# Performance work log

Hardware: AMD Instinct MI355X
Metric: run time of the kernel (lower is better)

Reference implementation:

```python
import jax, jax.numpy as jnp
import numpy as np

H, NH, NKV, HD, S, B = 4096, 32, 8, 128, 2048, 1
QMAX = 127.0  # int8 symmetric


def fake_quant(x, axis=None):
    """Symmetric int8 fake quantization with straight-through estimator.
    axis=None -> per-tensor dynamic scale; axis=int -> per-channel along that axis."""
    if axis is None:
        amax = jnp.max(jnp.abs(x))
    else:
        amax = jnp.max(jnp.abs(x), axis=axis, keepdims=True)
    scale = jnp.maximum(amax, 1e-8) / QMAX
    q = jnp.clip(jnp.round(x / scale), -QMAX - 1, QMAX) * scale
    return x + jax.lax.stop_gradient(q - x)


def quant_linear(x, w):
    # weight: per-output-channel quant (reduce over in-features axis=1);
    # activation: per-tensor dynamic quant
    xq = fake_quant(x)
    wq = fake_quant(w, axis=1)
    return jnp.einsum('bsh,oh->bso', xq, wq)


def rotate_half(x):
    x1, x2 = jnp.split(x, 2, axis=-1)
    return jnp.concatenate([-x2, x1], axis=-1)


def apply_rope(q, k, cos, sin):
    # q: [B,NH,S,HD], k: [B,NKV,S,HD], cos/sin: [B,S,HD]
    cos = cos[:, None, :, :]
    sin = sin[:, None, :, :]
    return q * cos + rotate_half(q) * sin, k * cos + rotate_half(k) * sin


def setup_inputs() -> dict:
    key = jax.random.key(0)
    ks = jax.random.split(key, 6)
    hidden_states = jax.random.normal(ks[0], (B, S, H), jnp.float32)
    # additive causal mask
    neg = jnp.finfo(jnp.float32).min
    mask = jnp.where(jnp.tril(jnp.ones((S, S), bool)), 0.0, neg)
    attention_mask = jnp.broadcast_to(mask, (B, 1, S, S)).astype(jnp.float32)
    # rotary cos/sin
    inv_freq = 1.0 / (10000.0 ** (jnp.arange(0, HD, 2, dtype=jnp.float32) / HD))
    t = jnp.arange(S, dtype=jnp.float32)
    freqs = jnp.outer(t, inv_freq)                     # [S, HD/2]
    emb = jnp.concatenate([freqs, freqs], axis=-1)     # [S, HD]
    cos = jnp.broadcast_to(jnp.cos(emb), (B, S, HD))
    sin = jnp.broadcast_to(jnp.sin(emb), (B, S, HD))
    sc = 0.02
    wq = jax.random.normal(ks[1], (H, H), jnp.float32) * sc
    wk = jax.random.normal(ks[2], (NKV * HD, H), jnp.float32) * sc
    wv = jax.random.normal(ks[3], (NKV * HD, H), jnp.float32) * sc
    wo = jax.random.normal(ks[4], (H, H), jnp.float32) * sc
    return {"hidden_states": hidden_states, "attention_mask": attention_mask,
            "cos": cos, "sin": sin, "wq": wq, "wk": wk, "wv": wv, "wo": wo}


def reference(hidden_states, attention_mask, cos, sin, wq, wk, wv, wo):
    b, s, _ = hidden_states.shape
    scaling = HD ** -0.5
    q = quant_linear(hidden_states, wq).reshape(b, s, NH, HD).transpose(0, 2, 1, 3)
    k = quant_linear(hidden_states, wk).reshape(b, s, NKV, HD).transpose(0, 2, 1, 3)
    v = quant_linear(hidden_states, wv).reshape(b, s, NKV, HD).transpose(0, 2, 1, 3)
    q, k = apply_rope(q, k, cos, sin)
    groups = NH // NKV
    k = jnp.repeat(k, groups, axis=1)  # [B,NH,S,HD]
    v = jnp.repeat(v, groups, axis=1)
    # quantize before QK^T
    qq = fake_quant(q)
    kq = fake_quant(k)
    attn = jnp.einsum('bhqd,bhkd->bhqk', qq, kq) * scaling
    attn = attn + attention_mask
    attn = jnp.maximum(attn, jnp.finfo(attn.dtype).min)
    attn = jax.nn.softmax(attn.astype(jnp.float32), axis=-1).astype(q.dtype)
    # quantize before PV
    pq = fake_quant(attn)
    vq = fake_quant(v)
    out = jnp.einsum('bhqk,bhkd->bhqd', pq, vq)
    out = out.transpose(0, 2, 1, 3).reshape(b, s, NH * HD)
    out = quant_linear(out, wo)
    return out
```

## Files before the change

### kernel.cpp

```cpp
#include <hip/hip_runtime.h>
#include <cstdint>
#include <cstddef>


#define S_LEN   2048
#define HDIM    4096
#define NHEADS  32
#define NKVH    8
#define HEADD   128
#define QMAXF   127.0f
#define ROPE_BLOCKS 20480

typedef _Float16 half8  __attribute__((ext_vector_type(8)));
typedef float    floatx4 __attribute__((ext_vector_type(4)));

__device__ __forceinline__ float wave_max64(float v){
#pragma unroll
  for (int off = 32; off > 0; off >>= 1) v = fmaxf(v, __shfl_xor(v, off));
  return v;
}
__device__ __forceinline__ float grp16_max(float v){
#pragma unroll
  for (int off = 8; off > 0; off >>= 1) v = fmaxf(v, __shfl_xor(v, off));
  return v;
}
__device__ __forceinline__ float grp16_sum(float v){
#pragma unroll
  for (int off = 8; off > 0; off >>= 1) v += __shfl_xor(v, off);
  return v;
}
__device__ __forceinline__ void atomic_max_f(unsigned* p, float v){
  atomicMax(p, __float_as_uint(v));
}
__device__ __forceinline__ float q8(float x, float scale){
  return fminf(fmaxf(rintf(x / scale), -128.f), 127.f);
}
__device__ __forceinline__ void gload_lds16(const _Float16* g, _Float16* l){
  __builtin_amdgcn_global_load_lds((const __attribute__((address_space(1))) void*)g,
                                   (__attribute__((address_space(3))) void*)l, 16, 0, 0);
}

__device__ __forceinline__ void block_atomic_max(float m, unsigned* out){
  m = wave_max64(m);
  __shared__ float red[4];
  int wid = threadIdx.x >> 6;
  if ((threadIdx.x & 63) == 0) red[wid] = m;
  __syncthreads();
  if (threadIdx.x == 0)
    atomic_max_f(out, fmaxf(fmaxf(red[0], red[1]), fmaxf(red[2], red[3])));
}

__global__ void k_init(float* scal){ if (threadIdx.x < 16) scal[threadIdx.x] = 0.0f; }

__global__ void k_amax(const float* __restrict__ x, size_t n4, unsigned* __restrict__ out){
  size_t i = (size_t)blockIdx.x * blockDim.x + threadIdx.x;
  size_t stride = (size_t)gridDim.x * blockDim.x;
  float m = 0.f;
  for (; i < n4; i += stride){
    float4 v = ((const float4*)x)[i];
    m = fmaxf(m, fmaxf(fmaxf(fabsf(v.x), fabsf(v.y)), fmaxf(fabsf(v.z), fabsf(v.w))));
  }
  block_atomic_max(m, out);
}

__global__ void k_amax_v(const float* __restrict__ Y, unsigned* __restrict__ out){
  size_t i = (size_t)blockIdx.x * blockDim.x + threadIdx.x;
  size_t stride = (size_t)gridDim.x * blockDim.x;
  float m = 0.f;
  for (size_t e = i; e < (size_t)S_LEN * 1024; e += stride){
    size_t s = e >> 10; int c = (int)(e & 1023);
    m = fmaxf(m, fabsf(Y[s * 6144 + 5120 + c]));
  }
  block_atomic_max(m, out);
}

__global__ void k_quant(const float* __restrict__ x, _Float16* __restrict__ q,
                        size_t n4, const float* __restrict__ amax){
  float scale = fmaxf(*amax, 1e-8f) / QMAXF;
  size_t i = (size_t)blockIdx.x * blockDim.x + threadIdx.x;
  size_t stride = (size_t)gridDim.x * blockDim.x;
  for (; i < n4; i += stride){
    float4 v = ((const float4*)x)[i];
    union { _Float16 h[4]; uint2 u; } pk;
    pk.h[0] = (_Float16)q8(v.x, scale);
    pk.h[1] = (_Float16)q8(v.y, scale);
    pk.h[2] = (_Float16)q8(v.z, scale);
    pk.h[3] = (_Float16)q8(v.w, scale);
    ((uint2*)q)[i] = pk.u;
  }
}

__global__ __launch_bounds__(256) void k_quant_w(
    const float* __restrict__ wq, const float* __restrict__ wk,
    const float* __restrict__ wv, const float* __restrict__ wo,
    _Float16* __restrict__ Wall, _Float16* __restrict__ Wo,
    float* __restrict__ wsc)
{
  int row = blockIdx.x;
  const float* src; _Float16* dst;
  if (row < 4096)      { src = wq + (size_t)row * HDIM;          dst = Wall + (size_t)row * HDIM; }
  else if (row < 5120) { src = wk + (size_t)(row - 4096) * HDIM; dst = Wall + (size_t)row * HDIM; }
  else if (row < 6144) { src = wv + (size_t)(row - 5120) * HDIM; dst = Wall + (size_t)row * HDIM; }
  else                 { src = wo + (size_t)(row - 6144) * HDIM; dst = Wo + (size_t)(row - 6144) * HDIM; }
  float4 v[4]; float m = 0.f;
#pragma unroll
  for (int i = 0; i < 4; i++){
    v[i] = ((const float4*)src)[threadIdx.x + i * 256];
    m = fmaxf(m, fmaxf(fmaxf(fabsf(v[i].x), fabsf(v[i].y)), fmaxf(fabsf(v[i].z), fabsf(v[i].w))));
  }
  m = wave_max64(m);
  __shared__ float red[4];
  int wid = threadIdx.x >> 6;
  if ((threadIdx.x & 63) == 0) red[wid] = m;
  __syncthreads();
  float am = fmaxf(fmaxf(red[0], red[1]), fmaxf(red[2], red[3]));
  float scale = fmaxf(am, 1e-8f) / QMAXF;
  if (threadIdx.x == 0) wsc[row] = scale;
#pragma unroll
  for (int i = 0; i < 4; i++){
    union { _Float16 h[4]; uint2 u; } pk;
    pk.h[0] = (_Float16)q8(v[i].x, scale);
    pk.h[1] = (_Float16)q8(v[i].y, scale);
    pk.h[2] = (_Float16)q8(v[i].z, scale);
    pk.h[3] = (_Float16)q8(v[i].w, scale);
    ((uint2*)dst)[threadIdx.x + i * 256] = pk.u;
  }
}

__global__ __launch_bounds__(256) void k_rope(
    float* __restrict__ Y, const float* __restrict__ cosb,
    const float* __restrict__ sinb,
    float* __restrict__ qpart, float* __restrict__ kpart)
{
  int idx = blockIdx.x * 256 + threadIdx.x;
  int s = idx / (40 * 64);
  int rem = idx - s * 40 * 64;
  int head = rem >> 6;
  int d = rem & 63;
  size_t base = (size_t)s * 6144 + (head < 32 ? head * 128 : 4096 + (head - 32) * 128);
  float x1 = Y[base + d], x2 = Y[base + d + 64];
  float c1 = cosb[s * 128 + d],      s1 = sinb[s * 128 + d];
  float c2 = cosb[s * 128 + d + 64], s2 = sinb[s * 128 + d + 64];
  float o1 = x1 * c1 - x2 * s1;
  float o2 = x2 * c2 + x1 * s2;
  Y[base + d] = o1; Y[base + d + 64] = o2;
  float m = wave_max64(fmaxf(fabsf(o1), fabsf(o2)));
  __shared__ float wmax[4]; __shared__ int wisq[4];
  int wid = threadIdx.x >> 6;
  if ((threadIdx.x & 63) == 0){ wmax[wid] = m; wisq[wid] = (head < 32); }
  __syncthreads();
  if (threadIdx.x == 0){
    float qm = 0.f, km = 0.f;
#pragma unroll
    for (int w = 0; w < 4; w++){
      if (wisq[w]) qm = fmaxf(qm, wmax[w]); else km = fmaxf(km, wmax[w]);
    }
    qpart[blockIdx.x] = qm; kpart[blockIdx.x] = km;
  }
}

__global__ __launch_bounds__(256) void k_reduce_qk(
    const float* __restrict__ qpart, const float* __restrict__ kpart,
    float* __restrict__ scal)
{
  const float* src = blockIdx.x ? kpart : qpart;
  float m = 0.f;
  for (int i = threadIdx.x; i < ROPE_BLOCKS; i += 256) m = fmaxf(m, src[i]);
  m = wave_max64(m);
  __shared__ float red[4];
  int wid = threadIdx.x >> 6;
  if ((threadIdx.x & 63) == 0) red[wid] = m;
  __syncthreads();
  if (threadIdx.x == 0)
    scal[1 + blockIdx.x] = fmaxf(fmaxf(red[0], red[1]), fmaxf(red[2], red[3]));
}

__global__ __launch_bounds__(256) void k_quant_qk(
    const float* __restrict__ Y, _Float16* __restrict__ Qh,
    _Float16* __restrict__ Kh, const float* __restrict__ scal)
{
  int i = blockIdx.x * 256 + threadIdx.x;
  int s = i / 1280, c4 = i - s * 1280;
  int col = c4 * 4;
  float4 v = *(const float4*)(Y + (size_t)s * 6144 + col);
  float scale = fmaxf(col < 4096 ? scal[1] : scal[2], 1e-8f) / QMAXF;
  union { _Float16 h[4]; uint2 u; } pk;
  pk.h[0] = (_Float16)q8(v.x, scale);
  pk.h[1] = (_Float16)q8(v.y, scale);
  pk.h[2] = (_Float16)q8(v.z, scale);
  pk.h[3] = (_Float16)q8(v.w, scale);
  if (col < 4096) *(uint2*)(Qh + (size_t)s * 4096 + col) = pk.u;
  else            *(uint2*)(Kh + (size_t)s * 1024 + (col - 4096)) = pk.u;
}

__global__ __launch_bounds__(256) void k_quant_vt(
    const float* __restrict__ Y, _Float16* __restrict__ Vt,
    const float* __restrict__ scal)
{
  __shared__ _Float16 sT[64][72];
  const int s0 = blockIdx.x * 64, kvh = blockIdx.y, dh = blockIdx.z;
  const float scale = fmaxf(scal[3], 1e-8f) / QMAXF;
  const int d = threadIdx.x & 63, srow = threadIdx.x >> 6;
#pragma unroll
  for (int i = 0; i < 16; i++){
    int s = srow + i * 4;
    float v = Y[(size_t)(s0 + s) * 6144 + 5120 + kvh * 128 + dh * 64 + d];
    sT[d][s] = (_Float16)q8(v, scale);
  }
  __syncthreads();
  const int dr = threadIdx.x >> 2, j = threadIdx.x & 3;
  _Float16* dst = Vt + (size_t)kvh * HEADD * S_LEN + (size_t)(dh * 64 + dr) * S_LEN + s0 + j * 16;
  *(uint4*)(dst)     = *(const uint4*)(&sT[dr][j * 16]);
  *(uint4*)(dst + 8) = *(const uint4*)(&sT[dr][j * 16 + 8]);
}

__global__ __launch_bounds__(256) void k_gemm_nt(
    const _Float16* __restrict__ A, const _Float16* __restrict__ B,
    const float* __restrict__ amax_a, const float* __restrict__ sb,
    float* __restrict__ C, int M, int N, int K)
{
  __shared__ _Float16 sA[128 * 32];
  __shared__ _Float16 sB[128 * 32];
  const int m0 = blockIdx.x * 128;
  const int n0 = blockIdx.y * 128;
  const int tid = threadIdx.x;
  const int w = tid >> 6, lane = tid & 63;
  const int quad = lane >> 4, l16 = lane & 15;
  const int wm = (w & 1) * 64, wn = (w >> 1) * 64;
  floatx4 acc[4][4] = {};
  const int srow = w * 16 + (lane >> 2);
  const int scol = (lane & 3) * 8;
  const _Float16* gA0 = A + (size_t)(m0 + srow) * K + scol;
  const _Float16* gA1 = A + (size_t)(m0 + 64 + srow) * K + scol;
  const _Float16* gB0 = B + (size_t)(n0 + srow) * K + scol;
  const _Float16* gB1 = B + (size_t)(n0 + 64 + srow) * K + scol;
  _Float16* dA0 = sA + w * 512 + lane * 8;
  _Float16* dA1 = sA + 2048 + w * 512 + lane * 8;
  _Float16* dB0 = sB + w * 512 + lane * 8;
  _Float16* dB1 = sB + 2048 + w * 512 + lane * 8;

  for (int k0 = 0; k0 < K; k0 += 32){
    __syncthreads();
    gload_lds16(gA0 + k0, dA0);
    gload_lds16(gA1 + k0, dA1);
    gload_lds16(gB0 + k0, dB0);
    gload_lds16(gB1 + k0, dB1);
    __syncthreads();
    half8 af[4], bf[4];
#pragma unroll
    for (int i = 0; i < 4; i++){
      af[i] = *(const half8*)(sA + (wm + i * 16 + l16) * 32 + quad * 8);
      bf[i] = *(const half8*)(sB + (wn + i * 16 + l16) * 32 + quad * 8);
    }
#pragma unroll
    for (int i = 0; i < 4; i++)
#pragma unroll
      for (int j = 0; j < 4; j++)
        acc[i][j] = __builtin_amdgcn_mfma_f32_16x16x32_f16(af[i], bf[j], acc[i][j], 0, 0, 0);
  }
  const float sa = fmaxf(*amax_a, 1e-8f) / QMAXF;
#pragma unroll
  for (int i = 0; i < 4; i++){
    int row = m0 + wm + i * 16 + quad * 4;
#pragma unroll
    for (int j = 0; j < 4; j++){
      int col = n0 + wn + j * 16 + l16;
      float sc2 = sa * sb[col];
#pragma unroll
      for (int rr = 0; rr < 4; rr++)
        C[(size_t)(row + rr) * N + col] = acc[i][j][rr] * sc2;
    }
  }
}

__global__ __launch_bounds__(256) void k_attn(
    const _Float16* __restrict__ Qh,
    const _Float16* __restrict__ Kh,
    const _Float16* __restrict__ Vt,
    const float* __restrict__ scal,
    float* __restrict__ AO)
{
  const int h   = blockIdx.y;
  const int kvh = h >> 2;
  const int tid = threadIdx.x;
  const int wid = tid >> 6, lane = tid & 63;
  const int quad = lane >> 4, l16 = lane & 15;

  __shared__ _Float16 sK[64 * 136];
  __shared__ _Float16 sV[128 * 72];
  __shared__ _Float16 sP[4][16 * 72];

  const float s_q = fmaxf(scal[1], 1e-8f) / QMAXF;
  const float s_k = fmaxf(scal[2], 1e-8f) / QMAXF;
  const float s_v = fmaxf(scal[3], 1e-8f) / QMAXF;
  const float qkscale = s_q * s_k * 0.08838834764831845f;
  const float osc = s_v * (1.0f / QMAXF);

  for (int half = 0; half < 2; half++){
    const int qb = half ? (31 - blockIdx.x) : blockIdx.x;
    const int qrow = qb * 64 + wid * 16 + l16;
    half8 qf[4];
#pragma unroll
    for (int kk = 0; kk < 4; kk++)
      qf[kk] = *(const half8*)(Qh + (size_t)qrow * 4096 + h * 128 + kk * 32 + quad * 8);
    const int q_of_reg = qb * 64 + wid * 16 + quad * 4;

    float mrow[4] = { -__builtin_inff(), -__builtin_inff(), -__builtin_inff(), -__builtin_inff() };
    float lrow[4] = { 0.f, 0.f, 0.f, 0.f };

    for (int kt = 0; kt <= qb; ++kt){
      int r = tid >> 2, seg = tid & 3;
      const uint4* gK = (const uint4*)(Kh + (size_t)(kt * 64 + r) * 1024 + kvh * 128 + seg * 32);
      uint4 t0 = gK[0], t1 = gK[1], t2 = gK[2], t3 = gK[3];
      __syncthreads();
      { uint4* d1 = (uint4*)(sK + r * 136 + seg * 32); d1[0] = t0; d1[1] = t1; d1[2] = t2; d1[3] = t3; }
      __syncthreads();
      float sv[4][4];
      const bool diag = (kt == qb);
#pragma unroll
      for (int nt = 0; nt < 4; nt++){
        floatx4 c = {};
#pragma unroll
        for (int kk = 0; kk < 4; kk++){
          half8 bf = *(const half8*)(sK + (nt * 16 + l16) * 136 + kk * 32 + quad * 8);
          c = __builtin_amdgcn_mfma_f32_16x16x32_f16(qf[kk], bf, c, 0, 0, 0);
        }
        if (diag){
          int kpos = kt * 64 + nt * 16 + l16;
#pragma unroll
          for (int rr = 0; rr < 4; rr++)
            sv[nt][rr] = (kpos <= q_of_reg + rr) ? c[rr] * qkscale : -__builtin_inff();
        } else {
#pragma unroll
          for (int rr = 0; rr < 4; rr++) sv[nt][rr] = c[rr] * qkscale;
        }
      }
#pragma unroll
      for (int rr = 0; rr < 4; rr++){
        float lmax = fmaxf(fmaxf(sv[0][rr], sv[1][rr]), fmaxf(sv[2][rr], sv[3][rr]));
        float tmax = grp16_max(lmax);
        float mnew = fmaxf(mrow[rr], tmax);
        float lsum = 0.f;
#pragma unroll
        for (int nt = 0; nt < 4; nt++) lsum += __expf(sv[nt][rr] - mnew);
        lsum = grp16_sum(lsum);
        lrow[rr] = lrow[rr] * __expf(mrow[rr] - mnew) + lsum;
        mrow[rr] = mnew;
      }
    }

    float il[4];
#pragma unroll
    for (int rr = 0; rr < 4; rr++) il[rr] = QMAXF * __builtin_amdgcn_rcpf(lrow[rr]);

    floatx4 accO[8] = {};
    for (int kt = 0; kt <= qb; ++kt){
      int r = tid >> 2, seg = tid & 3;
      const uint4* gK = (const uint4*)(Kh + (size_t)(kt * 64 + r) * 1024 + kvh * 128 + seg * 32);
      uint4 t0 = gK[0], t1 = gK[1], t2 = gK[2], t3 = gK[3];
      int vr = tid >> 1, vh = tid & 1;
      const uint4* gV = (const uint4*)(Vt + (size_t)kvh * HEADD * S_LEN + (size_t)vr * S_LEN + kt * 64 + vh * 32);
      uint4 u0 = gV[0], u1 = gV[1], u2 = gV[2], u3 = gV[3];
      __syncthreads();
      { uint4* d1 = (uint4*)(sK + r * 136 + seg * 32); d1[0] = t0; d1[1] = t1; d1[2] = t2; d1[3] = t3; }
      { uint4* d2 = (uint4*)(sV + vr * 72 + vh * 32);  d2[0] = u0; d2[1] = u1; d2[2] = u2; d2[3] = u3; }
      __syncthreads();
      const bool diag = (kt == qb);
#pragma unroll
      for (int nt = 0; nt < 4; nt++){
        floatx4 c = {};
#pragma unroll
        for (int kk = 0; kk < 4; kk++){
          half8 bf = *(const half8*)(sK + (nt * 16 + l16) * 136 + kk * 32 + quad * 8);
          c = __builtin_amdgcn_mfma_f32_16x16x32_f16(qf[kk], bf, c, 0, 0, 0);
        }
        int kpos = kt * 64 + nt * 16 + l16;
#pragma unroll
        for (int rr = 0; rr < 4; rr++){
          float pq = fminf(rintf(__expf(c[rr] * qkscale - mrow[rr]) * il[rr]), 127.f);
          if (diag && kpos > q_of_reg + rr) pq = 0.f;
          sP[wid][(quad * 4 + rr) * 72 + nt * 16 + l16] = (_Float16)pq;
        }
      }
      __syncthreads();
      half8 pf0 = *(const half8*)(&sP[wid][l16 * 72 + quad * 8]);
      half8 pf1 = *(const half8*)(&sP[wid][l16 * 72 + 32 + quad * 8]);
#pragma unroll
      for (int dt = 0; dt < 8; dt++){
        half8 b0 = *(const half8*)(sV + (dt * 16 + l16) * 72 + quad * 8);
        half8 b1 = *(const half8*)(sV + (dt * 16 + l16) * 72 + 32 + quad * 8);
        accO[dt] = __builtin_amdgcn_mfma_f32_16x16x32_f16(pf0, b0, accO[dt], 0, 0, 0);
        accO[dt] = __builtin_amdgcn_mfma_f32_16x16x32_f16(pf1, b1, accO[dt], 0, 0, 0);
      }
    }

#pragma unroll
    for (int dt = 0; dt < 8; dt++){
      int col = h * 128 + dt * 16 + l16;
#pragma unroll
      for (int rr = 0; rr < 4; rr++)
        AO[(size_t)(q_of_reg + rr) * 4096 + col] = accO[dt][rr] * osc;
    }
  }
}

extern "C" void kernel_launch(void* const* d_in, const int* in_sizes, int n_in,
                              void* d_out, int out_size, void* d_ws, size_t ws_size,
                              hipStream_t stream)
{
  const float* hidden = (const float*)d_in[0];
  const float* cosb = (const float*)d_in[2];
  const float* sinb = (const float*)d_in[3];
  const float* wq = (const float*)d_in[4];
  const float* wk = (const float*)d_in[5];
  const float* wv = (const float*)d_in[6];
  const float* wo = (const float*)d_in[7];
  float* out = (float*)d_out;

  char* ws = (char*)d_ws;
  size_t off = 0;
  auto alloc = [&](size_t bytes){ size_t o = off; off += (bytes + 255) & ~(size_t)255; return o; };
  float*    scal  = (float*)   (ws + alloc(64));
  float*    wsc   = (float*)   (ws + alloc(10240 * 4));
  float*    qpart = (float*)   (ws + alloc(ROPE_BLOCKS * 4));
  float*    kpart = (float*)   (ws + alloc(ROPE_BLOCKS * 4));
  _Float16* Wall  = (_Float16*)(ws + alloc((size_t)6144 * 4096 * 2));
  _Float16* Wo    = (_Float16*)(ws + alloc((size_t)4096 * 4096 * 2));
  _Float16* Xq    = (_Float16*)(ws + alloc((size_t)2048 * 4096 * 2));
  float*    Y     = (float*)   (ws + alloc((size_t)2048 * 6144 * 4));
  _Float16* Qh  = Xq;
  _Float16* Kh  = Wall;
  _Float16* Vt  = Wall + (size_t)2048 * 1024;
  float*    AO  = Y;
  _Float16* AOq = (_Float16*)((char*)Y + (size_t)2048 * 4096 * 4);

  unsigned* su = (unsigned*)scal;

  k_init<<<dim3(1), dim3(64), 0, stream>>>(scal);
  k_quant_w<<<dim3(10240), dim3(256), 0, stream>>>(wq, wk, wv, wo, Wall, Wo, wsc);
  k_amax<<<dim3(256), dim3(256), 0, stream>>>(hidden, (size_t)(2048 * 4096 / 4), su + 0);
  k_quant<<<dim3(2048), dim3(256), 0, stream>>>(hidden, Xq, (size_t)(2048 * 4096 / 4), scal + 0);
  k_gemm_nt<<<dim3(16, 48), dim3(256), 0, stream>>>(Xq, Wall, scal + 0, wsc, Y, 2048, 6144, 4096);
  k_rope<<<dim3(ROPE_BLOCKS), dim3(256), 0, stream>>>(Y, cosb, sinb, qpart, kpart);
  k_reduce_qk<<<dim3(2), dim3(256), 0, stream>>>(qpart, kpart, scal);
  k_amax_v<<<dim3(256), dim3(256), 0, stream>>>(Y, su + 3);
  k_quant_qk<<<dim3(10240), dim3(256), 0, stream>>>(Y, Qh, Kh, scal);
  k_quant_vt<<<dim3(32, 8, 2), dim3(256), 0, stream>>>(Y, Vt, scal);
  k_attn<<<dim3(16, 32), dim3(256), 0, stream>>>(Qh, Kh, Vt, scal, AO);
  k_amax<<<dim3(256), dim3(256), 0, stream>>>(AO, (size_t)(2048 * 4096 / 4), su + 4);
  k_quant<<<dim3(2048), dim3(256), 0, stream>>>(AO, AOq, (size_t)(2048 * 4096 / 4), scal + 4);
  k_gemm_nt<<<dim3(16, 32), dim3(256), 0, stream>>>(AOq, Wo, scal + 4, wsc + 6144, out, 2048, 4096, 4096);
}
```

Before: 683.9 us.

## Restructure attention: two heads per block, transposed MFMA, double-buffered K/V prefetch

The attention kernel now has each block process two query heads that share one KV head, so each K/V tile loaded into shared memory is reused for both heads. The QK product is computed transposed (K as the A operand), which leaves P in registers in the layout the 16x16x16 PV MFMA expects and removes the sP shared-memory round trip and its extra barrier. Row reductions use cross-quad shuffles, and K/V tiles are double-buffered with register prefetch of the next tile. The grid is halved, and register pressure roughly doubles for accumulators, with launch bounds asking for 2 blocks per CU.

```diff
diff --git a/kernel.cpp b/kernel.cpp
--- a/kernel.cpp
+++ b/kernel.cpp
@@ -12,21 +12,12 @@
 #define ROPE_BLOCKS 20480
 
 typedef _Float16 half8  __attribute__((ext_vector_type(8)));
+typedef _Float16 half4  __attribute__((ext_vector_type(4)));
 typedef float    floatx4 __attribute__((ext_vector_type(4)));
 
 __device__ __forceinline__ float wave_max64(float v){
 #pragma unroll
   for (int off = 32; off > 0; off >>= 1) v = fmaxf(v, __shfl_xor(v, off));
-  return v;
-}
-__device__ __forceinline__ float grp16_max(float v){
-#pragma unroll
-  for (int off = 8; off > 0; off >>= 1) v = fmaxf(v, __shfl_xor(v, off));
-  return v;
-}
-__device__ __forceinline__ float grp16_sum(float v){
-#pragma unroll
-  for (int off = 8; off > 0; off >>= 1) v += __shfl_xor(v, off);
   return v;
 }
 __device__ __forceinline__ void atomic_max_f(unsigned* p, float v){
@@ -273,134 +264,182 @@
   }
 }
 
-__global__ __launch_bounds__(256) void k_attn(
+__global__ __launch_bounds__(256, 2) void k_attn(
     const _Float16* __restrict__ Qh,
     const _Float16* __restrict__ Kh,
     const _Float16* __restrict__ Vt,
     const float* __restrict__ scal,
     float* __restrict__ AO)
 {
-  const int h   = blockIdx.y;
-  const int kvh = h >> 2;
+  const int h0  = blockIdx.y * 2;
+  const int kvh = h0 >> 2;
   const int tid = threadIdx.x;
   const int wid = tid >> 6, lane = tid & 63;
   const int quad = lane >> 4, l16 = lane & 15;
 
-  __shared__ _Float16 sK[64 * 136];
-  __shared__ _Float16 sV[128 * 72];
-  __shared__ _Float16 sP[4][16 * 72];
+  __shared__ _Float16 sK[2][64 * 136];
+  __shared__ _Float16 sV[2][128 * 72];
 
   const float s_q = fmaxf(scal[1], 1e-8f) / QMAXF;
   const float s_k = fmaxf(scal[2], 1e-8f) / QMAXF;
   const float s_v = fmaxf(scal[3], 1e-8f) / QMAXF;
   const float qkscale = s_q * s_k * 0.08838834764831845f;
   const float osc = s_v * (1.0f / QMAXF);
-
-  for (int half = 0; half < 2; half++){
-    const int qb = half ? (31 - blockIdx.x) : blockIdx.x;
+  const float NEGINF = -__builtin_inff();
+
+  const int kr_ = tid >> 2, ks_ = tid & 3;
+  const int vr_ = tid >> 1, vh_ = tid & 1;
+  const _Float16* gK0 = Kh + (size_t)kr_ * 1024 + kvh * 128 + ks_ * 32;
+  const _Float16* gV0 = Vt + (size_t)kvh * HEADD * S_LEN + (size_t)vr_ * S_LEN + vh_ * 32;
+
+  for (int hf = 0; hf < 2; hf++){
+    const int qb = hf ? 31 - (int)blockIdx.x : (int)blockIdx.x;
+    const int nk = qb + 1;
     const int qrow = qb * 64 + wid * 16 + l16;
-    half8 qf[4];
-#pragma unroll
-    for (int kk = 0; kk < 4; kk++)
-      qf[kk] = *(const half8*)(Qh + (size_t)qrow * 4096 + h * 128 + kk * 32 + quad * 8);
-    const int q_of_reg = qb * 64 + wid * 16 + quad * 4;
-
-    float mrow[4] = { -__builtin_inff(), -__builtin_inff(), -__builtin_inff(), -__builtin_inff() };
-    float lrow[4] = { 0.f, 0.f, 0.f, 0.f };
-
-    for (int kt = 0; kt <= qb; ++kt){
-      int r = tid >> 2, seg = tid & 3;
-      const uint4* gK = (const uint4*)(Kh + (size_t)(kt * 64 + r) * 1024 + kvh * 128 + seg * 32);
-      uint4 t0 = gK[0], t1 = gK[1], t2 = gK[2], t3 = gK[3];
+    const int qloc = wid * 16 + l16;
+
+    half8 qf[2][4];
+#pragma unroll
+    for (int hh = 0; hh < 2; hh++)
+#pragma unroll
+      for (int kk = 0; kk < 4; kk++)
+        qf[hh][kk] = *(const half8*)(Qh + (size_t)qrow * 4096 + (h0 + hh) * 128 + kk * 32 + quad * 8);
+
+    float mh[2] = { NEGINF, NEGINF };
+    float lh[2] = { 0.f, 0.f };
+
+    uint4 kpre[4];
+    {
+      const uint4* g = (const uint4*)gK0;
+#pragma unroll
+      for (int j = 0; j < 4; j++) kpre[j] = g[j];
+    }
+    __syncthreads();
+    for (int kt = 0; kt < nk; ++kt){
+      const int b = kt & 1;
+      { uint4* d = (uint4*)(sK[b] + kr_ * 136 + ks_ * 32);
+#pragma unroll
+        for (int j = 0; j < 4; j++) d[j] = kpre[j]; }
       __syncthreads();
-      { uint4* d1 = (uint4*)(sK + r * 136 + seg * 32); d1[0] = t0; d1[1] = t1; d1[2] = t2; d1[3] = t3; }
+      if (kt + 1 < nk){
+        const uint4* g = (const uint4*)(gK0 + (size_t)(kt + 1) * 65536);
+#pragma unroll
+        for (int j = 0; j < 4; j++) kpre[j] = g[j];
+      }
+      const bool diag = (kt == qb);
+      floatx4 c0[4], c1[4];
+#pragma unroll
+      for (int mt = 0; mt < 4; mt++){
+        c0[mt] = (floatx4){0.f,0.f,0.f,0.f}; c1[mt] = (floatx4){0.f,0.f,0.f,0.f};
+#pragma unroll
+        for (int kk = 0; kk < 4; kk++){
+          half8 a = *(const half8*)(sK[b] + (mt * 16 + l16) * 136 + kk * 32 + quad * 8);
+          c0[mt] = __builtin_amdgcn_mfma_f32_16x16x32_f16(a, qf[0][kk], c0[mt], 0, 0, 0);
+          c1[mt] = __builtin_amdgcn_mfma_f32_16x16x32_f16(a, qf[1][kk], c1[mt], 0, 0, 0);
+        }
+      }
+#pragma unroll
+      for (int mt = 0; mt < 4; mt++)
+#pragma unroll
+        for (int rr = 0; rr < 4; rr++){
+          bool ok = !diag || (mt * 16 + quad * 4 + rr <= qloc);
+          c0[mt][rr] = ok ? c0[mt][rr] * qkscale : NEGINF;
+          c1[mt][rr] = ok ? c1[mt][rr] * qkscale : NEGINF;
+        }
+#pragma unroll
+      for (int hh = 0; hh < 2; hh++){
+        floatx4* c = hh ? c1 : c0;
+        float vmax = NEGINF;
+#pragma unroll
+        for (int mt = 0; mt < 4; mt++)
+#pragma unroll
+          for (int rr = 0; rr < 4; rr++) vmax = fmaxf(vmax, c[mt][rr]);
+        vmax = fmaxf(vmax, __shfl_xor(vmax, 16));
+        vmax = fmaxf(vmax, __shfl_xor(vmax, 32));
+        float mnew = fmaxf(mh[hh], vmax);
+        float sum = 0.f;
+#pragma unroll
+        for (int mt = 0; mt < 4; mt++)
+#pragma unroll
+          for (int rr = 0; rr < 4; rr++) sum += __expf(c[mt][rr] - mnew);
+        sum += __shfl_xor(sum, 16);
+        sum += __shfl_xor(sum, 32);
+        lh[hh] = lh[hh] * __expf(mh[hh] - mnew) + sum;
+        mh[hh] = mnew;
+      }
+    }
+    float il[2] = { QMAXF * __builtin_amdgcn_rcpf(lh[0]),
+                    QMAXF * __builtin_amdgcn_rcpf(lh[1]) };
+
+    floatx4 accO[2][8] = {};
+    uint4 kpre2[4], vpre2[4];
+    {
+      const uint4* g = (const uint4*)gK0;
+      const uint4* v = (const uint4*)gV0;
+#pragma unroll
+      for (int j = 0; j < 4; j++){ kpre2[j] = g[j]; vpre2[j] = v[j]; }
+    }
+    __syncthreads();
+    for (int kt = 0; kt < nk; ++kt){
+      const int b = kt & 1;
+      { uint4* d = (uint4*)(sK[b] + kr_ * 136 + ks_ * 32);
+        uint4* e = (uint4*)(sV[b] + vr_ * 72 + vh_ * 32);
+#pragma unroll
+        for (int j = 0; j < 4; j++){ d[j] = kpre2[j]; e[j] = vpre2[j]; } }
       __syncthreads();
-      float sv[4][4];
+      if (kt + 1 < nk){
+        const uint4* g = (const uint4*)(gK0 + (size_t)(kt + 1) * 65536);
+        const uint4* v = (const uint4*)(gV0 + (kt + 1) * 64);
+#pragma unroll
+        for (int j = 0; j < 4; j++){ kpre2[j] = g[j]; vpre2[j] = v[j]; }
+      }
       const bool diag = (kt == qb);
-#pragma unroll
-      for (int nt = 0; nt < 4; nt++){
-        floatx4 c = {};
+      floatx4 c0[4], c1[4];
+#pragma unroll
+      for (int mt = 0; mt < 4; mt++){
+        c0[mt] = (floatx4){0.f,0.f,0.f,0.f}; c1[mt] = (floatx4){0.f,0.f,0.f,0.f};
 #pragma unroll
         for (int kk = 0; kk < 4; kk++){
-          half8 bf = *(const half8*)(sK + (nt * 16 + l16) * 136 + kk * 32 + quad * 8);
-          c = __builtin_amdgcn_mfma_f32_16x16x32_f16(qf[kk], bf, c, 0, 0, 0);
+          half8 a = *(const half8*)(sK[b] + (mt * 16 + l16) * 136 + kk * 32 + quad * 8);
+          c0[mt] = __builtin_amdgcn_mfma_f32_16x16x32_f16(a, qf[0][kk], c0[mt], 0, 0, 0);
+          c1[mt] = __builtin_amdgcn_mfma_f32_16x16x32_f16(a, qf[1][kk], c1[mt], 0, 0, 0);
         }
-        if (diag){
-          int kpos = kt * 64 + nt * 16 + l16;
-#pragma unroll
-          for (int rr = 0; rr < 4; rr++)
-            sv[nt][rr] = (kpos <= q_of_reg + rr) ? c[rr] * qkscale : -__builtin_inff();
-        } else {
-#pragma unroll
-          for (int rr = 0; rr < 4; rr++) sv[nt][rr] = c[rr] * qkscale;
+      }
+      half4 pk[2][4];
+#pragma unroll
+      for (int hh = 0; hh < 2; hh++){
+        floatx4* c = hh ? c1 : c0;
+#pragma unroll
+        for (int mt = 0; mt < 4; mt++){
+          half4 p;
+#pragma unroll
+          for (int rr = 0; rr < 4; rr++){
+            bool ok = !diag || (mt * 16 + quad * 4 + rr <= qloc);
+            float s = ok ? c[mt][rr] * qkscale : NEGINF;
+            float pq = fminf(rintf(__expf(s - mh[hh]) * il[hh]), 127.f);
+            p[rr] = (_Float16)pq;
+          }
+          pk[hh][mt] = p;
         }
       }
 #pragma unroll
-      for (int rr = 0; rr < 4; rr++){
-        float lmax = fmaxf(fmaxf(sv[0][rr], sv[1][rr]), fmaxf(sv[2][rr], sv[3][rr]));
-        float tmax = grp16_max(lmax);
-        float mnew = fmaxf(mrow[rr], tmax);
-        float lsum = 0.f;
-#pragma unroll
-        for (int nt = 0; nt < 4; nt++) lsum += __expf(sv[nt][rr] - mnew);
-        lsum = grp16_sum(lsum);
-        lrow[rr] = lrow[rr] * __expf(mrow[rr] - mnew) + lsum;
-        mrow[rr] = mnew;
-      }
-    }
-
-    float il[4];
-#pragma unroll
-    for (int rr = 0; rr < 4; rr++) il[rr] = QMAXF * __builtin_amdgcn_rcpf(lrow[rr]);
-
-    floatx4 accO[8] = {};
-    for (int kt = 0; kt <= qb; ++kt){
-      int r = tid >> 2, seg = tid & 3;
-      const uint4* gK = (const uint4*)(Kh + (size_t)(kt * 64 + r) * 1024 + kvh * 128 + seg * 32);
-      uint4 t0 = gK[0], t1 = gK[1], t2 = gK[2], t3 = gK[3];
-      int vr = tid >> 1, vh = tid & 1;
-      const uint4* gV = (const uint4*)(Vt + (size_t)kvh * HEADD * S_LEN + (size_t)vr * S_LEN + kt * 64 + vh * 32);
-      uint4 u0 = gV[0], u1 = gV[1], u2 = gV[2], u3 = gV[3];
-      __syncthreads();
-      { uint4* d1 = (uint4*)(sK + r * 136 + seg * 32); d1[0] = t0; d1[1] = t1; d1[2] = t2; d1[3] = t3; }
-      { uint4* d2 = (uint4*)(sV + vr * 72 + vh * 32);  d2[0] = u0; d2[1] = u1; d2[2] = u2; d2[3] = u3; }
-      __syncthreads();
-      const bool diag = (kt == qb);
-#pragma unroll
-      for (int nt = 0; nt < 4; nt++){
-        floatx4 c = {};
-#pragma unroll
-        for (int kk = 0; kk < 4; kk++){
-          half8 bf = *(const half8*)(sK + (nt * 16 + l16) * 136 + kk * 32 + quad * 8);
-          c = __builtin_amdgcn_mfma_f32_16x16x32_f16(qf[kk], bf, c, 0, 0, 0);
+      for (int mt = 0; mt < 4; mt++)
+#pragma unroll
+        for (int dt = 0; dt < 8; dt++){
+          half4 va = *(const half4*)(sV[b] + (dt * 16 + l16) * 72 + mt * 16 + quad * 4);
+          accO[0][dt] = __builtin_amdgcn_mfma_f32_16x16x16f16(va, pk[0][mt], accO[0][dt], 0, 0, 0);
+          accO[1][dt] = __builtin_amdgcn_mfma_f32_16x16x16f16(va, pk[1][mt], accO[1][dt], 0, 0, 0);
         }
-        int kpos = kt * 64 + nt * 16 + l16;
-#pragma unroll
-        for (int rr = 0; rr < 4; rr++){
-          float pq = fminf(rintf(__expf(c[rr] * qkscale - mrow[rr]) * il[rr]), 127.f);
-          if (diag && kpos > q_of_reg + rr) pq = 0.f;
-          sP[wid][(quad * 4 + rr) * 72 + nt * 16 + l16] = (_Float16)pq;
-        }
-      }
-      __syncthreads();
-      half8 pf0 = *(const half8*)(&sP[wid][l16 * 72 + quad * 8]);
-      half8 pf1 = *(const half8*)(&sP[wid][l16 * 72 + 32 + quad * 8]);
+    }
+
+#pragma unroll
+    for (int hh = 0; hh < 2; hh++)
 #pragma unroll
       for (int dt = 0; dt < 8; dt++){
-        half8 b0 = *(const half8*)(sV + (dt * 16 + l16) * 72 + quad * 8);
-        half8 b1 = *(const half8*)(sV + (dt * 16 + l16) * 72 + 32 + quad * 8);
-        accO[dt] = __builtin_amdgcn_mfma_f32_16x16x32_f16(pf0, b0, accO[dt], 0, 0, 0);
-        accO[dt] = __builtin_amdgcn_mfma_f32_16x16x32_f16(pf1, b1, accO[dt], 0, 0, 0);
-      }
-    }
-
-#pragma unroll
-    for (int dt = 0; dt < 8; dt++){
-      int col = h * 128 + dt * 16 + l16;
-#pragma unroll
-      for (int rr = 0; rr < 4; rr++)
-        AO[(size_t)(q_of_reg + rr) * 4096 + col] = accO[dt][rr] * osc;
-    }
+        float4 o = { accO[hh][dt][0] * osc, accO[hh][dt][1] * osc,
+                     accO[hh][dt][2] * osc, accO[hh][dt][3] * osc };
+        *(float4*)(AO + (size_t)qrow * 4096 + (h0 + hh) * 128 + dt * 16 + quad * 4) = o;
+      }
   }
 }
 
@@ -446,7 +485,7 @@
   k_amax_v<<<dim3(256), dim3(256), 0, stream>>>(Y, su + 3);
   k_quant_qk<<<dim3(10240), dim3(256), 0, stream>>>(Y, Qh, Kh, scal);
   k_quant_vt<<<dim3(32, 8, 2), dim3(256), 0, stream>>>(Y, Vt, scal);
-  k_attn<<<dim3(16, 32), dim3(256), 0, stream>>>(Qh, Kh, Vt, scal, AO);
+  k_attn<<<dim3(16, 16), dim3(256), 0, stream>>>(Qh, Kh, Vt, scal, AO);
   k_amax<<<dim3(256), dim3(256), 0, stream>>>(AO, (size_t)(2048 * 4096 / 4), su + 4);
   k_quant<<<dim3(2048), dim3(256), 0, stream>>>(AO, AOq, (size_t)(2048 * 4096 / 4), scal + 4);
   k_gemm_nt<<<dim3(16, 32), dim3(256), 0, stream>>>(AOq, Wo, scal + 4, wsc + 6144, out, 2048, 4096, 4096);
```

Result: slower. 716.4 us (+4.8%).
